# Kernel optimization log

Hardware: AMD Instinct MI355X
Metric: run time of the kernel (lower is better)

Reference implementation:

```python
import jax, jax.numpy as jnp
import numpy as np

PAD = 2  # kernel_height // 2 for kernel_height=5


def earth_pad2d(x, ph, pw):
    # circular pad in longitude (last dim), zero pad in latitude (dim 2)
    if pw > 0:
        x = jnp.concatenate([x[..., -pw:], x, x[..., :pw]], axis=-1)
    if ph > 0:
        x = jnp.pad(x, ((0, 0), (0, 0), (ph, ph), (0, 0)))
    return x


def earth_wrap2d(x, w, pad):
    # fold circular overhang of a transposed-conv output back onto width w
    core = x[..., pad:pad + w]
    rw = x.shape[-1] - pad - w  # right overhang (stride-1... here 1)
    core = core.at[..., :rw].add(x[..., pad + w:])
    core = core.at[..., w - pad:].add(x[..., :pad])
    return core


def _conv(x, w, b, stride):
    # torch Conv2d, weight [Cout, Cin, 1, k], VALID padding, stride (1, stride)
    y = jax.lax.conv_general_dilated(x, w, (1, stride), 'VALID',
                                     dimension_numbers=('NCHW', 'OIHW', 'NCHW'))
    return y + b[None, :, None, None]


def _convT(x, w, stride):
    # torch ConvTranspose2d (no bias), weight [Cin, Cout, 1, k], padding 0
    k = w.shape[-1]
    wr = jnp.transpose(jnp.flip(w, axis=(2, 3)), (1, 0, 2, 3))  # -> [Cout, Cin, 1, k]
    return jax.lax.conv_general_dilated(x, wr, (1, 1),
                                        [(0, 0), (k - 1, k - 1)],
                                        lhs_dilation=(1, stride),
                                        dimension_numbers=('NCHW', 'OIHW', 'NCHW'))


def _edge(x, d, p):
    return x[:, :, -p:, :] if d == 1 else x[:, :, :p, :]


def _set_edge(x, d, p, v):
    return x.at[:, :, -p:, :].set(v) if d == 1 else x.at[:, :, :p, :].set(v)


def _forward(strips, wi, wo):
    strips_pad = [earth_pad2d(s, PAD, PAD) for s in strips]
    # center strip inner edges from the adjacent coarser strips (to_inners[0])
    for d in (-1, 1):
        a = _edge(strips[2 + d], -d, PAD)
        a = _convT(a, wi[0], 2)
        a = earth_wrap2d(a, strips[2].shape[3], 2)
        a = earth_pad2d(a, 0, PAD)
        strips_pad[2] = _set_edge(strips_pad[2], d, PAD, a)
    # outer strips: far edge from next coarser (to_inners), near edge from finer (to_outers)
    for mi in (1, 2):
        for d in (-1, 1):
            idx = 2 + d * mi
            sp = strips_pad[idx]
            if mi + 1 <= 2:
                o = _edge(strips[2 + d * (mi + 1)], -d, PAD)
                o = _convT(o, wi[mi], 2)
                o = earth_wrap2d(o, strips[idx].shape[3], 2)
                o = earth_pad2d(o, 0, PAD)
                sp = _set_edge(sp, d, PAD, o)
            en = _edge(strips[2 + d * (mi - 1)], d, PAD)
            en = earth_pad2d(en, 0, 2)
            en = _conv(en, wo[mi - 1][0], wo[mi - 1][1], 2)
            en = earth_pad2d(en, 0, PAD)
            sp = _set_edge(sp, -d, PAD, en)
            strips_pad[idx] = sp
    return tuple(strips_pad)


def setup_inputs():
    key = jax.random.key(0)
    ks = jax.random.split(key, 11)
    B, C, W = 1, 256, 1440
    shapes = [(B, C, 30, W // 4), (B, C, 60, W // 2), (B, C, 180, W),
              (B, C, 60, W // 2), (B, C, 30, W // 4)]
    d = {}
    for i, sh in enumerate(shapes):
        d['s%d' % i] = jax.random.normal(ks[i], sh, dtype=jnp.float32)
    scale = 0.03
    d['wi0'] = jax.random.normal(ks[5], (C, C, 1, 5), dtype=jnp.float32) * scale
    d['wi1'] = jax.random.normal(ks[6], (C, C, 1, 5), dtype=jnp.float32) * scale
    d['wo0'] = jax.random.normal(ks[7], (C, C, 1, 5), dtype=jnp.float32) * scale
    d['bo0'] = jax.random.normal(ks[8], (C,), dtype=jnp.float32) * 0.01
    d['wo1'] = jax.random.normal(ks[9], (C, C, 1, 5), dtype=jnp.float32) * scale
    d['bo1'] = jax.random.normal(ks[10], (C,), dtype=jnp.float32) * 0.01
    return d


def reference(s0, s1, s2, s3, s4, wi0, wi1, wo0, bo0, wo1, bo1):
    return _forward([s0, s1, s2, s3, s4], [wi0, wi1], [(wo0, bo0), (wo1, bo1)])
```

## Files before the change

kernel.cpp:

```cpp
#include <hip/hip_runtime.h>


struct ConvJob {
  const float* x; const float* wt; const float* bias; float* out;
  int Hin, Win, r0, Hout, Wcore, h0, type, blk_start;
};

struct MegaParams {
  ConvJob j[8];
  const float* in0; const float* in1; const float* in2; const float* in3; const float* in4;
  float* o0; float* o1; float* o2; float* o3; float* o4;
};

struct WTParams { const float* src[4]; float* dst[4]; };

__global__ __launch_bounds__(256) void transpose_all_kernel(WTParams p) {
  int b = blockIdx.x;
  int which = b / 1280;
  int idx = (b - which * 1280) * 256 + threadIdx.x;
  int oc = idx & 255;
  int q = idx >> 8;
  int k = q % 5;
  int ic = q / 5;
  const float* s = p.src[which];
  float v = (which < 2) ? s[(ic * 256 + oc) * 5 + k] : s[(oc * 256 + ic) * 5 + k];
  p.dst[which][idx] = v;
}

template <int H, int W>
__device__ __forceinline__ void copy_strip(const float* __restrict__ in,
                                           float* __restrict__ out, int id) {
  constexpr int WO4 = W / 4 + 1;
  int w4 = id % WO4;
  int hz = id / WO4;
  int h = hz % H;
  int c = hz / H;
  const float* src = in + ((size_t)(c * H + h)) * W;
  int wc = w4 * 4;
  float4 v;
  if (w4 >= 1 && wc <= W - 4) {
    float2 a = *(const float2*)(src + wc - 2);
    float2 b = *(const float2*)(src + wc);
    v = make_float4(a.x, a.y, b.x, b.y);
  } else {
    int c0 = wc - 2 + W;
    v.x = src[c0 % W];
    v.y = src[(c0 + 1) % W];
    v.z = src[(c0 + 2) % W];
    v.w = src[(c0 + 3) % W];
  }
  *(float4*)(out + ((size_t)(c * (H + 4) + h + 2)) * (W + 4) + wc) = v;
}

__device__ __forceinline__ void conv_block(const ConvJob jb, int local, int t, float* xs) {
  int tile = local >> 1;
  int r = local & 1;
  const int Win = jb.Win;
  const float* xrow = jb.x + ((size_t)(t * jb.Hin + jb.r0 + r)) * Win;
  const float* wt = jb.wt + t;
  const int Wop = jb.Wcore + 4;
  float* orow = jb.out + ((size_t)(t * jb.Hout + jb.h0 + r)) * Wop;

  if (jb.type == 1) {
    int u0 = tile * 8;
    int cb = 2 * u0 - 2;
#pragma unroll
    for (int cc = 0; cc < 19; ++cc) {
      int col = cb + cc;
      col += (col < 0) ? Win : 0;
      col -= (col >= Win) ? Win : 0;
      xs[cc * 256 + t] = xrow[col];
    }
    __syncthreads();
    float bv = jb.bias[t];
    float acc[8];
#pragma unroll
    for (int i = 0; i < 8; ++i) acc[i] = bv;
    for (int ic0 = 0; ic0 < 256; ic0 += 4) {
      float w[4][5];
#pragma unroll
      for (int i = 0; i < 4; ++i)
#pragma unroll
        for (int k = 0; k < 5; ++k) w[i][k] = wt[((ic0 + i) * 5 + k) * 256];
#pragma unroll
      for (int cc = 0; cc < 19; ++cc) {
        float4 xq = *(const float4*)&xs[cc * 256 + ic0];
#pragma unroll
        for (int i = 0; i < 8; ++i) {
          int k = cc - 2 * i;
          if (k >= 0 && k < 5)
            acc[i] += w[0][k] * xq.x + w[1][k] * xq.y + w[2][k] * xq.z + w[3][k] * xq.w;
        }
      }
    }
#pragma unroll
    for (int i = 0; i < 8; ++i) {
      int g = u0 + i;
      float vv = acc[i];
      orow[2 + g] = vv;
      if (g < 2) orow[jb.Wcore + 2 + g] = vv;
      if (g >= jb.Wcore - 2) orow[g - (jb.Wcore - 2)] = vv;
    }
  } else {
    int m0 = tile * 16;
    int j0 = (m0 >> 1) - 1;
#pragma unroll
    for (int cc = 0; cc < 10; ++cc) {
      int col = j0 + cc;
      col += (col < 0) ? Win : 0;
      col -= (col >= Win) ? Win : 0;
      xs[cc * 256 + t] = xrow[col];
    }
    __syncthreads();
    float acc[16];
#pragma unroll
    for (int i = 0; i < 16; ++i) acc[i] = 0.f;
    for (int ic0 = 0; ic0 < 256; ic0 += 4) {
      float w[4][5];
#pragma unroll
      for (int i = 0; i < 4; ++i)
#pragma unroll
        for (int k = 0; k < 5; ++k) w[i][k] = wt[((ic0 + i) * 5 + k) * 256];
#pragma unroll
      for (int cc = 0; cc < 10; ++cc) {
        float4 xq = *(const float4*)&xs[cc * 256 + ic0];
#pragma unroll
        for (int ml = 0; ml < 16; ++ml) {
          int k = ml + 4 - 2 * cc;
          if (k >= 0 && k < 5)
            acc[ml] += w[0][k] * xq.x + w[1][k] * xq.y + w[2][k] * xq.z + w[3][k] * xq.w;
        }
      }
    }
#pragma unroll
    for (int i = 0; i < 16; ++i) {
      int g = m0 + i;
      float vv = acc[i];
      orow[2 + g] = vv;
      if (g < 2) orow[jb.Wcore + 2 + g] = vv;
      if (g >= jb.Wcore - 2) orow[g - (jb.Wcore - 2)] = vv;
    }
  }
}

__global__ __launch_bounds__(256) void mega_kernel(MegaParams p) {
  __shared__ float xs[19 * 256];
  int bx = blockIdx.x;
  int t = threadIdx.x;
  if (bx < 1080) {
    int ji = 0;
#pragma unroll
    for (int i = 1; i < 8; ++i)
      if (bx >= p.j[i].blk_start) ji = i;
    conv_block(p.j[ji], bx - p.j[ji].blk_start, t, xs);
  } else if (bx < 3810) {
    copy_strip<30, 360>(p.in0, p.o0, (bx - 1080) * 256 + t);
  } else if (bx < 14670) {
    copy_strip<60, 720>(p.in1, p.o1, (bx - 3810) * 256 + t);
  } else if (bx < 79650) {
    copy_strip<180, 1440>(p.in2, p.o2, (bx - 14670) * 256 + t);
  } else if (bx < 90510) {
    copy_strip<60, 720>(p.in3, p.o3, (bx - 79650) * 256 + t);
  } else if (bx < 93240) {
    copy_strip<30, 360>(p.in4, p.o4, (bx - 90510) * 256 + t);
  } else {
    int id = (bx - 93240) * 256 + t;
    int w4 = id % 91;
    int t2 = id / 91;
    int strip = t2 >> 9;
    int cr = t2 & 511;
    int c = cr >> 1;
    int r = cr & 1;
    float* o = (strip == 0) ? p.o0 + ((size_t)(c * 34 + r)) * 364
                            : p.o4 + ((size_t)(c * 34 + 32 + r)) * 364;
    *(float4*)(o + w4 * 4) = make_float4(0.f, 0.f, 0.f, 0.f);
  }
}

extern "C" void kernel_launch(void* const* d_in, const int* in_sizes, int n_in,
                              void* d_out, int out_size, void* d_ws, size_t ws_size,
                              hipStream_t stream) {
  const float* s0 = (const float*)d_in[0];
  const float* s1 = (const float*)d_in[1];
  const float* s2 = (const float*)d_in[2];
  const float* s3 = (const float*)d_in[3];
  const float* s4 = (const float*)d_in[4];
  const float* wi0 = (const float*)d_in[5];
  const float* wi1 = (const float*)d_in[6];
  const float* wo0 = (const float*)d_in[7];
  const float* bo0 = (const float*)d_in[8];
  const float* wo1 = (const float*)d_in[9];
  const float* bo1 = (const float*)d_in[10];

  float* out = (float*)d_out;
  float* out0 = out;
  float* out1 = out + 3168256;
  float* out2 = out + 15030272;
  float* out3 = out + 83048448;
  float* out4 = out + 94910464;

  float* wt0 = (float*)d_ws;
  float* wt1 = wt0 + 327680;
  float* wt2 = wt1 + 327680;
  float* wt3 = wt2 + 327680;

  WTParams wp;
  wp.src[0] = wi0; wp.src[1] = wi1; wp.src[2] = wo0; wp.src[3] = wo1;
  wp.dst[0] = wt0; wp.dst[1] = wt1; wp.dst[2] = wt2; wp.dst[3] = wt3;
  transpose_all_kernel<<<5120, 256, 0, stream>>>(wp);

  MegaParams mp;
  mp.j[0] = {s1, wt0, nullptr, out2,  60,  720,  58, 184, 1440,   0, 0,   0};
  mp.j[1] = {s3, wt0, nullptr, out2,  60,  720,   0, 184, 1440, 182, 0, 180};
  mp.j[2] = {s0, wt1, nullptr, out1,  30,  360,  28,  64,  720,   0, 0, 360};
  mp.j[3] = {s4, wt1, nullptr, out3,  30,  360,   0,  64,  720,  62, 0, 450};
  mp.j[4] = {s2, wt2, bo0,     out1, 180, 1440,   0,  64,  720,  62, 1, 540};
  mp.j[5] = {s2, wt2, bo0,     out3, 180, 1440, 178,  64,  720,   0, 1, 720};
  mp.j[6] = {s1, wt3, bo1,     out0,  60,  720,   0,  34,  360,  32, 1, 900};
  mp.j[7] = {s3, wt3, bo1,     out4,  60,  720,  58,  34,  360,   0, 1, 990};
  mp.in0 = s0; mp.in1 = s1; mp.in2 = s2; mp.in3 = s3; mp.in4 = s4;
  mp.o0 = out0; mp.o1 = out1; mp.o2 = out2; mp.o3 = out3; mp.o4 = out4;

  mega_kernel<<<93604, 256, 0, stream>>>(mp);
}
```

Before: 348.5 us.

## Use persistent grid-stride row copies and pair conv tiles per block

```diff
diff --git a/kernel.cpp b/kernel.cpp
--- a/kernel.cpp
+++ b/kernel.cpp
@@ -28,28 +28,30 @@
 }
 
 template <int H, int W>
-__device__ __forceinline__ void copy_strip(const float* __restrict__ in,
-                                           float* __restrict__ out, int id) {
+__device__ __forceinline__ void copy_strip_rows(const float* __restrict__ in,
+                                                float* __restrict__ out,
+                                                int lb, int nb, int t) {
   constexpr int WO4 = W / 4 + 1;
-  int w4 = id % WO4;
-  int hz = id / WO4;
-  int h = hz % H;
-  int c = hz / H;
-  const float* src = in + ((size_t)(c * H + h)) * W;
-  int wc = w4 * 4;
-  float4 v;
-  if (w4 >= 1 && wc <= W - 4) {
-    float2 a = *(const float2*)(src + wc - 2);
-    float2 b = *(const float2*)(src + wc);
-    v = make_float4(a.x, a.y, b.x, b.y);
-  } else {
-    int c0 = wc - 2 + W;
-    v.x = src[c0 % W];
-    v.y = src[(c0 + 1) % W];
-    v.z = src[(c0 + 2) % W];
-    v.w = src[(c0 + 3) % W];
+  constexpr int NROWS = 256 * H;
+  int wave = t >> 6, lane = t & 63;
+  for (int row = lb * 4 + wave; row < NROWS; row += nb * 4) {
+    int c = row / H;
+    const float* src = in + (size_t)row * W;
+    float* dst = out + (size_t)(row + c * 4 + 2) * (W + 4);
+    for (int w4 = 1 + lane; w4 < WO4 - 1; w4 += 64) {
+      const float* p = src + w4 * 4;
+      float2 a = *(const float2*)(p - 2);
+      float2 b = *(const float2*)(p);
+      *(float4*)(dst + w4 * 4) = make_float4(a.x, a.y, b.x, b.y);
+    }
+    if (lane == 0) {
+      float2 E = *(const float2*)(src + W - 2);
+      float2 F = *(const float2*)(src);
+      float4 v = make_float4(E.x, E.y, F.x, F.y);
+      *(float4*)(dst) = v;
+      *(float4*)(dst + W) = v;
+    }
   }
-  *(float4*)(out + ((size_t)(c * (H + 4) + h + 2)) * (W + 4) + wc) = v;
 }
 
 __device__ __forceinline__ void conv_block(const ConvJob jb, int local, int t, float* xs) {
@@ -143,37 +145,44 @@
   }
 }
 
-__global__ __launch_bounds__(256) void mega_kernel(MegaParams p) {
+__device__ __forceinline__ void conv_dispatch(const MegaParams& p, int u, int t, float* xs) {
+  int ji = 0;
+#pragma unroll
+  for (int i = 1; i < 8; ++i)
+    if (u >= p.j[i].blk_start) ji = i;
+  conv_block(p.j[ji], u - p.j[ji].blk_start, t, xs);
+}
+
+__global__ __launch_bounds__(256, 7) void mega_kernel(MegaParams p) {
   __shared__ float xs[19 * 256];
   int bx = blockIdx.x;
   int t = threadIdx.x;
-  if (bx < 1080) {
-    int ji = 0;
-#pragma unroll
-    for (int i = 1; i < 8; ++i)
-      if (bx >= p.j[i].blk_start) ji = i;
-    conv_block(p.j[ji], bx - p.j[ji].blk_start, t, xs);
-  } else if (bx < 3810) {
-    copy_strip<30, 360>(p.in0, p.o0, (bx - 1080) * 256 + t);
-  } else if (bx < 14670) {
-    copy_strip<60, 720>(p.in1, p.o1, (bx - 3810) * 256 + t);
-  } else if (bx < 79650) {
-    copy_strip<180, 1440>(p.in2, p.o2, (bx - 14670) * 256 + t);
-  } else if (bx < 90510) {
-    copy_strip<60, 720>(p.in3, p.o3, (bx - 79650) * 256 + t);
-  } else if (bx < 93240) {
-    copy_strip<30, 360>(p.in4, p.o4, (bx - 90510) * 256 + t);
+  if (bx < 540) {
+    conv_dispatch(p, bx, t, xs);
+    __syncthreads();
+    conv_dispatch(p, bx + 540, t, xs);
+  } else if (bx < 1410) {
+    copy_strip_rows<180, 1440>(p.in2, p.o2, bx - 540, 870, t);
+  } else if (bx < 1556) {
+    copy_strip_rows<60, 720>(p.in1, p.o1, bx - 1410, 146, t);
+  } else if (bx < 1702) {
+    copy_strip_rows<60, 720>(p.in3, p.o3, bx - 1556, 146, t);
+  } else if (bx < 1740) {
+    copy_strip_rows<30, 360>(p.in0, p.o0, bx - 1702, 38, t);
+  } else if (bx < 1778) {
+    copy_strip_rows<30, 360>(p.in4, p.o4, bx - 1740, 38, t);
   } else {
-    int id = (bx - 93240) * 256 + t;
-    int w4 = id % 91;
-    int t2 = id / 91;
-    int strip = t2 >> 9;
-    int cr = t2 & 511;
-    int c = cr >> 1;
-    int r = cr & 1;
-    float* o = (strip == 0) ? p.o0 + ((size_t)(c * 34 + r)) * 364
-                            : p.o4 + ((size_t)(c * 34 + 32 + r)) * 364;
-    *(float4*)(o + w4 * 4) = make_float4(0.f, 0.f, 0.f, 0.f);
+    int lb = bx - 1778;
+    int wave = t >> 6, lane = t & 63;
+    for (int row = lb * 4 + wave; row < 1024; row += 24) {
+      int strip = row >> 9;
+      int cr = row & 511;
+      int c = cr >> 1, r = cr & 1;
+      float* dst = strip ? p.o4 + (size_t)(c * 34 + 32 + r) * 364
+                         : p.o0 + (size_t)(c * 34 + r) * 364;
+      for (int w4 = lane; w4 < 91; w4 += 64)
+        *(float4*)(dst + w4 * 4) = make_float4(0.f, 0.f, 0.f, 0.f);
+    }
   }
 }
 
@@ -221,5 +230,5 @@
   mp.in0 = s0; mp.in1 = s1; mp.in2 = s2; mp.in3 = s3; mp.in4 = s4;
   mp.o0 = out0; mp.o1 = out1; mp.o2 = out2; mp.o3 = out3; mp.o4 = out4;
 
-  mega_kernel<<<93604, 256, 0, stream>>>(mp);
-}
+  mega_kernel<<<1784, 256, 0, stream>>>(mp);
+}
```

Measured after the change: 312.0 us. -10.5%, faster.
